# Optimization experiments

Hardware: AMD Instinct MI355X
Metric: run time of the kernel (lower is better)

Reference implementation:

```python
import jax, jax.numpy as jnp
import numpy as np

B, T, W, E, H, EMB, NVOCAB, WIN = 256, 200, 200, 768, 256, 32, 201, 8


def setup_inputs() -> dict:
    key = jax.random.key(0)
    ks = jax.random.split(key, 12)
    s = 0.05
    inputs = jax.random.normal(ks[0], (B, T, E), jnp.float32)
    full_word_embeddings = jax.random.normal(ks[1], (B, W, E), jnp.float32)
    lengths = jax.random.randint(ks[2], (B,), T // 2, T + 1)
    fix = jax.random.randint(ks[3], (B, T), 1, NVOCAB)
    fix_seq = jnp.where(jnp.arange(T)[None, :] < lengths[:, None], fix, 0)
    emb_table = (jax.random.normal(ks[4], (NVOCAB, EMB)) * s).at[0].set(0.0)  # padding_idx=0
    W_ih = jax.random.normal(ks[5], (3 * H, E + EMB)) * s  # torch GRU layout, gates r,z,n
    W_hh = jax.random.normal(ks[6], (3 * H, H)) * s
    b_ih = jax.random.normal(ks[7], (3 * H,)) * s
    b_hh = jax.random.normal(ks[8], (3 * H,)) * s
    W_out = jax.random.normal(ks[9], (E, H)) * s  # output_layer: Linear(H, E)
    b_out = jnp.zeros((E,), jnp.float32)
    W_dur = jax.random.normal(ks[10], (1, H)) * s  # duration_layer: Linear(H, 1)
    b_dur = jnp.zeros((1,), jnp.float32)
    return {"inputs": inputs, "fix_seq": fix_seq, "full_word_embeddings": full_word_embeddings,
            "lengths": lengths, "expert_id": 0, "emb_table": emb_table,
            "W_ih": W_ih, "b_ih": b_ih, "W_hh": W_hh, "b_hh": b_hh,
            "W_out": W_out, "b_out": b_out, "W_dur": W_dur, "b_dur": b_dur}


def _gru(x, W_ih, b_ih, W_hh, b_hh, h_dim):
    # x: [B,T,I]. Precompute input projections once, scan over time.
    xg = jnp.einsum('bti,gi->btg', x, W_ih) + b_ih  # [B,T,3H]

    def step(h, xg_t):
        hg = h @ W_hh.T + b_hh
        xr, xz, xn = jnp.split(xg_t, 3, axis=-1)
        hr, hz, hn = jnp.split(hg, 3, axis=-1)
        r = jax.nn.sigmoid(xr + hr)
        z = jax.nn.sigmoid(xz + hz)
        n = jnp.tanh(xn + r * hn)
        h_new = (1.0 - z) * n + z * h
        return h_new, h_new

    h0 = jnp.zeros((x.shape[0], h_dim), x.dtype)
    _, outs = jax.lax.scan(step, h0, jnp.swapaxes(xg, 0, 1))
    return jnp.swapaxes(outs, 0, 1)  # [B,T,H]


def reference(inputs, fix_seq, full_word_embeddings, lengths, expert_id,
              emb_table, W_ih, b_ih, W_hh, b_hh, W_out, b_out, W_dur, b_dur):
    del expert_id  # weights of the selected expert are passed directly
    valid_mask = fix_seq != 0
    scan_emb = emb_table[fix_seq]  # [B,T,32]
    rnn_in = jnp.concatenate([inputs, scan_emb], axis=-1)
    outputs = _gru(rnn_in, W_ih, b_ih, W_hh, b_hh, W_hh.shape[1])  # [B,T,H]
    # pad_packed_sequence zeros outputs beyond each sequence length
    tmask = jnp.arange(outputs.shape[1])[None, :] < lengths[:, None]
    outputs = outputs * tmask[..., None].astype(outputs.dtype)
    # dot attention: proj then scores against word embeddings
    proj = outputs @ W_out.T + b_out  # [B,T,E]
    logits = jnp.einsum('bte,bwe->btw', proj, full_word_embeddings)
    # saccade window mask around current fixation position
    wpos = jnp.arange(full_word_embeddings.shape[1])[None, None, :]
    dist = jnp.abs(wpos - fix_seq[..., None])
    sacc = (dist <= WIN) & valid_mask[..., None]
    logits = jnp.where(sacc, logits, -1e9)
    word_mask = jnp.sum(jnp.abs(full_word_embeddings), axis=-1) != 0
    logits = jnp.where(word_mask[:, None, :], logits, -1e9)
    dur_pred = (outputs @ W_dur.T + b_dur)[..., 0]  # [B,T]
    return logits, dur_pred
```

## Files before the change

kernel.cpp:

```cpp
#include <hip/hip_runtime.h>
#include <hip/hip_bf16.h>

typedef __attribute__((ext_vector_type(8))) short bf16x8;
typedef __attribute__((ext_vector_type(4))) float f32x4;
typedef __attribute__((ext_vector_type(4))) int   i32x4;

#define NB 256
#define NT 200
#define NW 200
#define NE 768
#define NH 256
#define NEMB 32
#define KIN 800
#define G3H 768
#define MROWS 51200

__device__ __forceinline__ float bf2f(unsigned short h) {
    return __uint_as_float(((unsigned)h) << 16);
}
__device__ __forceinline__ unsigned short f2bf(float f) {
    unsigned u = __float_as_uint(f);
    u += 0x7fff + ((u >> 16) & 1);
    return (unsigned short)(u >> 16);
}
__device__ __forceinline__ float sigm(float x) { return 1.0f / (1.0f + __expf(-x)); }
__device__ __forceinline__ float tanh_fast(float x) {
    float e = __expf(2.0f * x);
    return 1.0f - 2.0f / (e + 1.0f);
}

#if __has_builtin(__builtin_amdgcn_sdot4)
__device__ __forceinline__ int SDOT4(int a, int b, int c) {
    return __builtin_amdgcn_sdot4(a, b, c, false);
}
#else
__device__ __forceinline__ int SDOT4(int a, int b, int c) {
    #pragma unroll
    for (int j = 0; j < 4; j++)
        c += (int)(signed char)(a >> (8 * j)) * (int)(signed char)(b >> (8 * j));
    return c;
}
#endif

__device__ __forceinline__ void gload16(const void* g, void* l) {
    __builtin_amdgcn_global_load_lds((const __attribute__((address_space(1))) unsigned int*)g,
                                     (__attribute__((address_space(3))) unsigned int*)l,
                                     16, 0, 0);
}

__global__ void prep1(const float* __restrict__ inputs, const int* __restrict__ fix_seq,
                      const float* __restrict__ emb, const float* __restrict__ Wih,
                      const float* __restrict__ Wout, const float* __restrict__ bih,
                      const float* __restrict__ bhh,
                      unsigned short* __restrict__ Abf, unsigned short* __restrict__ Wihbf,
                      unsigned short* __restrict__ Woutbf, float* __restrict__ biasC) {
    const long gid0 = (long)blockIdx.x * blockDim.x + threadIdx.x;
    if (gid0 < G3H) biasC[gid0] = bih[gid0] + (gid0 < 512 ? bhh[gid0] : 0.0f);
    const long NA = (long)MROWS * 100;
    const long NWU = 768L * 100;
    const long NOU = 768L * 32;
    const long total = NA + NWU + NOU;
    for (long u = gid0; u < total; u += (long)gridDim.x * blockDim.x) {
        bf16x8 v;
        unsigned short* dst;
        if (u < NA) {
            long row = u / 100;
            int c8 = (int)(u % 100) * 8;
            const float* s;
            if (c8 < NE) {
                s = inputs + row * NE + c8;
            } else {
                int fx = fix_seq[row];
                s = emb + (long)fx * NEMB + (c8 - NE);
            }
            #pragma unroll
            for (int j = 0; j < 8; j++) v[j] = (short)f2bf(s[j]);
            dst = Abf + row * KIN + c8;
        } else if (u < NA + NWU) {
            long u2 = u - NA;
            long row = u2 / 100;
            int c8 = (int)(u2 % 100) * 8;
            const float* s = Wih + row * KIN + c8;
            #pragma unroll
            for (int j = 0; j < 8; j++) v[j] = (short)f2bf(s[j]);
            dst = Wihbf + row * KIN + c8;
        } else {
            long u3 = u - NA - NWU;
            long row = u3 / 32;
            int c8 = (int)(u3 % 32) * 8;
            const float* s = Wout + row * NH + c8;
            #pragma unroll
            for (int j = 0; j < 8; j++) v[j] = (short)f2bf(s[j]);
            dst = Woutbf + row * NH + c8;
        }
        *(bf16x8*)dst = v;
    }
}

__global__ __launch_bounds__(256)
void gemm_bt128(const unsigned short* __restrict__ A,
                const unsigned short* __restrict__ Bw,
                const float* __restrict__ bias,
                unsigned short* __restrict__ Out,
                int M, int N, int K) {
    __shared__ unsigned short As[128 * 32];
    __shared__ unsigned short Bs[128 * 32];
    const int bid = (int)((blockIdx.x & 7) * (gridDim.x >> 3) + (blockIdx.x >> 3));
    const int nblk = N >> 7;
    const int m0 = (bid / nblk) << 7;
    const int n0 = (bid % nblk) << 7;
    const int tid = threadIdx.x;
    const int lane = tid & 63;
    const int wave = tid >> 6;
    const int wm = (wave >> 1) << 6;
    const int wn = (wave & 1) << 6;
    const int nk = K >> 5;

    const int srow = tid >> 2;
    const int sseg = (tid & 3) << 4;
    const char* gA0 = (const char*)(A + (long)(m0 + srow) * K) + sseg;
    const char* gA1 = (const char*)(A + (long)(m0 + 64 + srow) * K) + sseg;
    const char* gB0 = (const char*)(Bw + (long)(n0 + srow) * K) + sseg;
    const char* gB1 = (const char*)(Bw + (long)(n0 + 64 + srow) * K) + sseg;
    char* lA0 = (char*)As + wave * 1024;
    char* lA1 = (char*)As + 4096 + wave * 1024;
    char* lB0 = (char*)Bs + wave * 1024;
    char* lB1 = (char*)Bs + 4096 + wave * 1024;

    f32x4 acc[4][4] = {};

    for (int kt = 0; kt < nk; kt++) {
        __syncthreads();
        gload16(gA0 + kt * 64, lA0);
        gload16(gA1 + kt * 64, lA1);
        gload16(gB0 + kt * 64, lB0);
        gload16(gB1 + kt * 64, lB1);
        asm volatile("s_waitcnt vmcnt(0)" ::: "memory");
        __syncthreads();
        bf16x8 af[4], bfr[4];
        #pragma unroll
        for (int mi = 0; mi < 4; mi++)
            af[mi] = *(const bf16x8*)((const char*)As +
                        (wm + mi * 16 + (lane & 15)) * 64 + ((lane >> 4) << 4));
        #pragma unroll
        for (int ni = 0; ni < 4; ni++)
            bfr[ni] = *(const bf16x8*)((const char*)Bs +
                        (wn + ni * 16 + (lane & 15)) * 64 + ((lane >> 4) << 4));
        #pragma unroll
        for (int mi = 0; mi < 4; mi++)
            #pragma unroll
            for (int ni = 0; ni < 4; ni++)
                acc[mi][ni] = __builtin_amdgcn_mfma_f32_16x16x32_bf16(
                                  af[mi], bfr[ni], acc[mi][ni], 0, 0, 0);
    }
    #pragma unroll
    for (int ni = 0; ni < 4; ni++) {
        const int col = n0 + wn + ni * 16 + (lane & 15);
        const float bv = bias[col];
        #pragma unroll
        for (int mi = 0; mi < 4; mi++) {
            const int row = m0 + wm + mi * 16 + ((lane >> 4) << 2);
            #pragma unroll
            for (int r = 0; r < 4; r++)
                Out[(long)(row + r) * N + col] = f2bf(acc[mi][ni][r] + bv);
        }
    }
}

__global__ __launch_bounds__(512, 2)
__attribute__((amdgpu_waves_per_eu(2, 2)))
void gru_scan(const unsigned short* __restrict__ xg,
              const float* __restrict__ Whh,
              const float* __restrict__ bhh,
              const int* __restrict__ lengths,
              unsigned short* __restrict__ hout) {
    __shared__ __align__(16) unsigned char h8[2][256];
    const int tid = threadIdx.x;
    const int lane = tid & 63;
    const int wave = tid >> 6;
    const int b = blockIdx.x;
    const int col = wave * 32 + (lane & 31);
    const int kh = lane >> 5;

    int W[3][32];
    #pragma unroll
    for (int g = 0; g < 3; g++) {
        const float* wr = Whh + (long)(g * 256 + col) * NH + kh * 128;
        #pragma unroll
        for (int d = 0; d < 32; d++) {
            const float4 f = *(const float4*)(wr + d * 4);
            unsigned pack = 0;
            #pragma unroll
            for (int j = 0; j < 4; j++) {
                const float fv = j == 0 ? f.x : j == 1 ? f.y : j == 2 ? f.z : f.w;
                int wq = (int)rintf(fv * 400.0f);
                wq = wq > 127 ? 127 : (wq < -127 ? -127 : wq);
                pack |= ((unsigned)(wq & 0xff)) << (8 * j);
            }
            W[g][d] = (int)pack;
        }
    }
    const float bhn = bhh[512 + col];
    const int len = lengths[b];
    if (tid < 128) ((unsigned*)h8)[tid] = 0u;

    const unsigned short* xrow = xg + (long)b * NT * G3H;
    unsigned short xv0 = xrow[col], xv1 = xrow[256 + col], xv2 = xrow[512 + col];
    float hp = 0.0f;
    const float ISC = 1.0f / (400.0f * 127.0f);
    const bool wlo = (lane < 32);

    asm volatile("s_waitcnt lgkmcnt(0)" ::: "memory");
    __builtin_amdgcn_sched_barrier(0);
    __builtin_amdgcn_s_barrier();
    __builtin_amdgcn_sched_barrier(0);

    for (int t = 0; t < NT; t++) {
        const unsigned char* hb = h8[(t + 1) & 1] + kh * 128;
        int p0a = 0, p0b = 0, p1a = 0, p1b = 0, p2a = 0, p2b = 0;
        #pragma unroll
        for (int r = 0; r < 8; r++) {
            const i32x4 hv = *(const i32x4*)(hb + r * 16);
            p0a = SDOT4(hv[0], W[0][r * 4 + 0], p0a);
            p1a = SDOT4(hv[0], W[1][r * 4 + 0], p1a);
            p2a = SDOT4(hv[0], W[2][r * 4 + 0], p2a);
            p0b = SDOT4(hv[1], W[0][r * 4 + 1], p0b);
            p1b = SDOT4(hv[1], W[1][r * 4 + 1], p1b);
            p2b = SDOT4(hv[1], W[2][r * 4 + 1], p2b);
            p0a = SDOT4(hv[2], W[0][r * 4 + 2], p0a);
            p1a = SDOT4(hv[2], W[1][r * 4 + 2], p1a);
            p2a = SDOT4(hv[2], W[2][r * 4 + 2], p2a);
            p0b = SDOT4(hv[3], W[0][r * 4 + 3], p0b);
            p1b = SDOT4(hv[3], W[1][r * 4 + 3], p1b);
            p2b = SDOT4(hv[3], W[2][r * 4 + 3], p2b);
        }
        int p0 = p0a + p0b, p1 = p1a + p1b, p2 = p2a + p2b;
        p0 += __shfl_xor(p0, 32);
        p1 += __shfl_xor(p1, 32);
        p2 += __shfl_xor(p2, 32);
        const float r = sigm(bf2f(xv0) + (float)p0 * ISC);
        const float z = sigm(bf2f(xv1) + (float)p1 * ISC);
        const float n = tanh_fast(bf2f(xv2) + r * ((float)p2 * ISC + bhn));
        hp = (1.0f - z) * n + z * hp;
        if (wlo) {
            h8[t & 1][col] = (unsigned char)((int)rintf(hp * 127.0f) & 0xff);
            hout[((long)b * NT + t) * NH + col] = (t < len) ? f2bf(hp) : (unsigned short)0;
        }
        if (t + 1 < NT) {
            const unsigned short* xn = xrow + (long)(t + 1) * G3H;
            xv0 = xn[col]; xv1 = xn[256 + col]; xv2 = xn[512 + col];
        }
        asm volatile("s_waitcnt lgkmcnt(0)" ::: "memory");
        __builtin_amdgcn_sched_barrier(0);
        __builtin_amdgcn_s_barrier();
        __builtin_amdgcn_sched_barrier(0);
    }
}

__global__ void prep2(const float* __restrict__ fwe, unsigned short* __restrict__ fwebf,
                      unsigned char* __restrict__ wmask) {
    const int row = (int)((blockIdx.x * blockDim.x + threadIdx.x) >> 6);
    const int lane = threadIdx.x & 63;
    if (row >= MROWS) return;
    const float* s = fwe + (long)row * NE;
    unsigned short* d = fwebf + (long)row * NE;
    float asum = 0.0f;
    #pragma unroll
    for (int i = 0; i < 12; i++) {
        const float v = s[lane + i * 64];
        asum += fabsf(v);
        d[lane + i * 64] = f2bf(v);
    }
    #pragma unroll
    for (int off = 32; off >= 1; off >>= 1) asum += __shfl_xor(asum, off);
    if (lane == 0) wmask[row] = (asum != 0.0f) ? 1 : 0;
}

__global__ void logits_gemm(const unsigned short* __restrict__ Aproj,
                            const unsigned short* __restrict__ Bfwe,
                            const int* __restrict__ fix_seq,
                            const unsigned char* __restrict__ wmask,
                            float* __restrict__ out) {
    __shared__ unsigned short As[64 * 32];
    __shared__ unsigned short Bs[64 * 32];
    const int blk = blockIdx.x;
    const int b = blk >> 4;
    const int mt = (blk >> 2) & 3;
    const int ntile = blk & 3;
    const int t0 = mt << 6;
    const int w0 = ntile << 6;
    const int tid = threadIdx.x;
    const int lane = tid & 63;
    const int wave = tid >> 6;
    const int wm = (wave >> 1) << 5;
    const int wn = (wave & 1) << 5;

    const int srow = tid >> 2;
    const int sbyte = (tid & 3) << 4;
    const int tA = t0 + srow > 199 ? 199 : t0 + srow;
    const int wB = w0 + srow > 199 ? 199 : w0 + srow;
    const char* ga = (const char*)(Aproj + ((long)b * NT + tA) * NE) + sbyte;
    const char* gb = (const char*)(Bfwe + ((long)b * NW + wB) * NE) + sbyte;
    char* la = (char*)As + srow * 64 + sbyte;
    char* lb = (char*)Bs + srow * 64 + sbyte;

    f32x4 acc[2][2] = {};
    bf16x8 ra = *(const bf16x8*)(ga);
    bf16x8 rb = *(const bf16x8*)(gb);
    for (int kt = 0; kt < 24; kt++) {
        __syncthreads();
        *(bf16x8*)(la) = ra;
        *(bf16x8*)(lb) = rb;
        __syncthreads();
        if (kt < 23) {
            ra = *(const bf16x8*)(ga + (kt + 1) * 64);
            rb = *(const bf16x8*)(gb + (kt + 1) * 64);
        }
        bf16x8 af[2], bfr[2];
        #pragma unroll
        for (int mi = 0; mi < 2; mi++)
            af[mi] = *(const bf16x8*)((const char*)As +
                        (wm + mi * 16 + (lane & 15)) * 64 + ((lane >> 4) << 4));
        #pragma unroll
        for (int ni = 0; ni < 2; ni++)
            bfr[ni] = *(const bf16x8*)((const char*)Bs +
                        (wn + ni * 16 + (lane & 15)) * 64 + ((lane >> 4) << 4));
        #pragma unroll
        for (int mi = 0; mi < 2; mi++)
            #pragma unroll
            for (int ni = 0; ni < 2; ni++)
                acc[mi][ni] = __builtin_amdgcn_mfma_f32_16x16x32_bf16(
                                  af[mi], bfr[ni], acc[mi][ni], 0, 0, 0);
    }
    #pragma unroll
    for (int mi = 0; mi < 2; mi++) {
        #pragma unroll
        for (int r = 0; r < 4; r++) {
            const int t = t0 + wm + mi * 16 + ((lane >> 4) << 2) + r;
            if (t >= NT) continue;
            const int fx = fix_seq[b * NT + t];
            #pragma unroll
            for (int ni = 0; ni < 2; ni++) {
                const int w = w0 + wn + ni * 16 + (lane & 15);
                if (w >= NW) continue;
                int d = w - fx; d = d < 0 ? -d : d;
                const bool ok = (fx != 0) && (d <= 8) && (wmask[b * NW + w] != 0);
                out[(long)b * (NT * NW) + t * NW + w] = ok ? acc[mi][ni][r] : -1e9f;
            }
        }
    }
}

__global__ void dur_kernel(const unsigned short* __restrict__ hout,
                           const float* __restrict__ Wdur, const float* __restrict__ bdur,
                           float* __restrict__ out) {
    const int row = (int)((blockIdx.x * blockDim.x + threadIdx.x) >> 6);
    const int lane = threadIdx.x & 63;
    if (row >= MROWS) return;
    const unsigned short* hp = hout + (long)row * NH + lane * 4;
    const uint2 hv = *(const uint2*)hp;
    const float4 wv = *(const float4*)(Wdur + lane * 4);
    float s = bf2f((unsigned short)(hv.x & 0xffff)) * wv.x
            + bf2f((unsigned short)(hv.x >> 16)) * wv.y
            + bf2f((unsigned short)(hv.y & 0xffff)) * wv.z
            + bf2f((unsigned short)(hv.y >> 16)) * wv.w;
    #pragma unroll
    for (int off = 32; off >= 1; off >>= 1) s += __shfl_down(s, off);
    if (lane == 0) out[(long)NB * NT * NW + row] = s + bdur[0];
}

extern "C" void kernel_launch(void* const* d_in, const int* in_sizes, int n_in,
                              void* d_out, int out_size, void* d_ws, size_t ws_size,
                              hipStream_t stream) {
    (void)in_sizes; (void)n_in; (void)out_size; (void)ws_size;
    const float* inputs  = (const float*)d_in[0];
    const int*   fix_seq = (const int*)d_in[1];
    const float* fwe     = (const float*)d_in[2];
    const int*   lengths = (const int*)d_in[3];
    const float* emb     = (const float*)d_in[5];
    const float* Wih     = (const float*)d_in[6];
    const float* bih     = (const float*)d_in[7];
    const float* Whh     = (const float*)d_in[8];
    const float* bhh     = (const float*)d_in[9];
    const float* Wout    = (const float*)d_in[10];
    const float* bout    = (const float*)d_in[11];
    const float* Wdur    = (const float*)d_in[12];
    const float* bdur    = (const float*)d_in[13];
    float* out = (float*)d_out;

    char* ws = (char*)d_ws;
    unsigned short* Abf    = (unsigned short*)(ws);
    unsigned short* xgbf   = (unsigned short*)(ws + 81920000);
    unsigned short* hout   = (unsigned short*)(ws + 160563200);
    unsigned short* Wihbf  = (unsigned short*)(ws + 186777600);
    unsigned short* Woutbf = (unsigned short*)(ws + 188006400);
    unsigned char*  wmask  = (unsigned char*)(ws + 188399616);
    float*          biasC  = (float*)(ws + 188450816);
    unsigned short* projbf = Abf;
    unsigned short* fwebf  = xgbf;

    prep1<<<2048, 256, 0, stream>>>(inputs, fix_seq, emb, Wih, Wout, bih, bhh,
                                    Abf, Wihbf, Woutbf, biasC);
    gemm_bt128<<<400 * 6, 256, 0, stream>>>(Abf, Wihbf, biasC, xgbf, MROWS, G3H, KIN);
    gru_scan<<<256, 512, 0, stream>>>(xgbf, Whh, bhh, lengths, hout);
    gemm_bt128<<<400 * 6, 256, 0, stream>>>(hout, Woutbf, bout, projbf, MROWS, G3H, NH);
    prep2<<<12800, 256, 0, stream>>>(fwe, fwebf, wmask);
    logits_gemm<<<4096, 256, 0, stream>>>(projbf, fwebf, fix_seq, wmask, out);
    dur_kernel<<<12800, 256, 0, stream>>>(hout, Wdur, bdur, out);
}
```

Measured before the change: 559.4 us.

## Reassociate attention projection onto word embeddings to shrink logits GEMM K

Rewrites logits = (h·W_outᵀ + b_out)·fweᵀ as h·(fwe·W_out)ᵀ + fwe·b_out. A GEMM now projects the word embeddings into H=256 space (fwe·W_out, N=256, K=768) in place of projecting GRU outputs to E=768, and the bias term becomes a per-word dot product computed in prep2. The logits GEMM then runs over K=256 instead of 768 and loads its tiles with direct global-to-LDS copies. This cuts projection FLOPs and logits-GEMM traffic. The cost is a transposed W_out conversion, an extra dvec buffer, and a slightly different rounding path through bf16 G.

```diff
diff --git a/kernel.cpp b/kernel.cpp
--- a/kernel.cpp
+++ b/kernel.cpp
@@ -53,12 +53,14 @@
                       const float* __restrict__ Wout, const float* __restrict__ bih,
                       const float* __restrict__ bhh,
                       unsigned short* __restrict__ Abf, unsigned short* __restrict__ Wihbf,
-                      unsigned short* __restrict__ Woutbf, float* __restrict__ biasC) {
+                      unsigned short* __restrict__ WoutTbf, float* __restrict__ biasC,
+                      float* __restrict__ bias0) {
     const long gid0 = (long)blockIdx.x * blockDim.x + threadIdx.x;
     if (gid0 < G3H) biasC[gid0] = bih[gid0] + (gid0 < 512 ? bhh[gid0] : 0.0f);
+    if (gid0 < NH) bias0[gid0] = 0.0f;
     const long NA = (long)MROWS * 100;
     const long NWU = 768L * 100;
-    const long NOU = 768L * 32;
+    const long NOU = 256L * 96;
     const long total = NA + NWU + NOU;
     for (long u = gid0; u < total; u += (long)gridDim.x * blockDim.x) {
         bf16x8 v;
@@ -86,12 +88,12 @@
             dst = Wihbf + row * KIN + c8;
         } else {
             long u3 = u - NA - NWU;
-            long row = u3 / 32;
-            int c8 = (int)(u3 % 32) * 8;
-            const float* s = Wout + row * NH + c8;
-            #pragma unroll
-            for (int j = 0; j < 8; j++) v[j] = (short)f2bf(s[j]);
-            dst = Woutbf + row * NH + c8;
+            long row = u3 / 96;
+            int c8 = (int)(u3 % 96) * 8;
+            #pragma unroll
+            for (int j = 0; j < 8; j++)
+                v[j] = (short)f2bf(Wout[(long)(c8 + j) * NH + row]);
+            dst = WoutTbf + row * NE + c8;
         }
         *(bf16x8*)dst = v;
     }
@@ -257,30 +259,40 @@
     }
 }
 
-__global__ void prep2(const float* __restrict__ fwe, unsigned short* __restrict__ fwebf,
-                      unsigned char* __restrict__ wmask) {
+__global__ void prep2(const float* __restrict__ fwe, const float* __restrict__ bout,
+                      unsigned short* __restrict__ fwebf,
+                      unsigned char* __restrict__ wmask, float* __restrict__ dvec) {
     const int row = (int)((blockIdx.x * blockDim.x + threadIdx.x) >> 6);
     const int lane = threadIdx.x & 63;
     if (row >= MROWS) return;
     const float* s = fwe + (long)row * NE;
     unsigned short* d = fwebf + (long)row * NE;
-    float asum = 0.0f;
+    float asum = 0.0f, vdot = 0.0f;
     #pragma unroll
     for (int i = 0; i < 12; i++) {
         const float v = s[lane + i * 64];
         asum += fabsf(v);
+        vdot += v * bout[lane + i * 64];
         d[lane + i * 64] = f2bf(v);
     }
     #pragma unroll
-    for (int off = 32; off >= 1; off >>= 1) asum += __shfl_xor(asum, off);
-    if (lane == 0) wmask[row] = (asum != 0.0f) ? 1 : 0;
-}
-
-__global__ void logits_gemm(const unsigned short* __restrict__ Aproj,
-                            const unsigned short* __restrict__ Bfwe,
-                            const int* __restrict__ fix_seq,
-                            const unsigned char* __restrict__ wmask,
-                            float* __restrict__ out) {
+    for (int off = 32; off >= 1; off >>= 1) {
+        asum += __shfl_xor(asum, off);
+        vdot += __shfl_xor(vdot, off);
+    }
+    if (lane == 0) {
+        wmask[row] = (asum != 0.0f) ? 1 : 0;
+        dvec[row] = vdot;
+    }
+}
+
+__global__ __launch_bounds__(256)
+void logits_gemm(const unsigned short* __restrict__ Hrow,
+                 const unsigned short* __restrict__ G,
+                 const int* __restrict__ fix_seq,
+                 const unsigned char* __restrict__ wmask,
+                 const float* __restrict__ dvec,
+                 float* __restrict__ out) {
     __shared__ unsigned short As[64 * 32];
     __shared__ unsigned short Bs[64 * 32];
     const int blk = blockIdx.x;
@@ -296,26 +308,21 @@
     const int wn = (wave & 1) << 5;
 
     const int srow = tid >> 2;
-    const int sbyte = (tid & 3) << 4;
+    const int sseg = (tid & 3) << 4;
     const int tA = t0 + srow > 199 ? 199 : t0 + srow;
     const int wB = w0 + srow > 199 ? 199 : w0 + srow;
-    const char* ga = (const char*)(Aproj + ((long)b * NT + tA) * NE) + sbyte;
-    const char* gb = (const char*)(Bfwe + ((long)b * NW + wB) * NE) + sbyte;
-    char* la = (char*)As + srow * 64 + sbyte;
-    char* lb = (char*)Bs + srow * 64 + sbyte;
+    const char* ga = (const char*)(Hrow + ((long)b * NT + tA) * NH) + sseg;
+    const char* gb = (const char*)(G + ((long)b * NW + wB) * NH) + sseg;
+    char* la = (char*)As + wave * 1024;
+    char* lb = (char*)Bs + wave * 1024;
 
     f32x4 acc[2][2] = {};
-    bf16x8 ra = *(const bf16x8*)(ga);
-    bf16x8 rb = *(const bf16x8*)(gb);
-    for (int kt = 0; kt < 24; kt++) {
+    for (int kt = 0; kt < 8; kt++) {
         __syncthreads();
-        *(bf16x8*)(la) = ra;
-        *(bf16x8*)(lb) = rb;
+        gload16(ga + kt * 64, la);
+        gload16(gb + kt * 64, lb);
+        asm volatile("s_waitcnt vmcnt(0)" ::: "memory");
         __syncthreads();
-        if (kt < 23) {
-            ra = *(const bf16x8*)(ga + (kt + 1) * 64);
-            rb = *(const bf16x8*)(gb + (kt + 1) * 64);
-        }
         bf16x8 af[2], bfr[2];
         #pragma unroll
         for (int mi = 0; mi < 2; mi++)
@@ -345,7 +352,8 @@
                 if (w >= NW) continue;
                 int d = w - fx; d = d < 0 ? -d : d;
                 const bool ok = (fx != 0) && (d <= 8) && (wmask[b * NW + w] != 0);
-                out[(long)b * (NT * NW) + t * NW + w] = ok ? acc[mi][ni][r] : -1e9f;
+                out[(long)b * (NT * NW) + t * NW + w] =
+                    ok ? acc[mi][ni][r] + dvec[b * NW + w] : -1e9f;
             }
         }
     }
@@ -389,22 +397,24 @@
     float* out = (float*)d_out;
 
     char* ws = (char*)d_ws;
-    unsigned short* Abf    = (unsigned short*)(ws);
-    unsigned short* xgbf   = (unsigned short*)(ws + 81920000);
-    unsigned short* hout   = (unsigned short*)(ws + 160563200);
-    unsigned short* Wihbf  = (unsigned short*)(ws + 186777600);
-    unsigned short* Woutbf = (unsigned short*)(ws + 188006400);
-    unsigned char*  wmask  = (unsigned char*)(ws + 188399616);
-    float*          biasC  = (float*)(ws + 188450816);
-    unsigned short* projbf = Abf;
-    unsigned short* fwebf  = xgbf;
+    unsigned short* Abf     = (unsigned short*)(ws);
+    unsigned short* xgbf    = (unsigned short*)(ws + 81920000);
+    unsigned short* hout    = (unsigned short*)(ws + 160563200);
+    unsigned short* Wihbf   = (unsigned short*)(ws + 186777600);
+    unsigned short* WoutTbf = (unsigned short*)(ws + 188006400);
+    unsigned char*  wmask   = (unsigned char*)(ws + 188399616);
+    float*          biasC   = (float*)(ws + 188450816);
+    float*          dvec    = (float*)(ws + 188453888);
+    float*          bias0   = (float*)(ws + 188658688);
+    unsigned short* fwebf   = Abf;
+    unsigned short* Gbf     = xgbf;
 
     prep1<<<2048, 256, 0, stream>>>(inputs, fix_seq, emb, Wih, Wout, bih, bhh,
-                                    Abf, Wihbf, Woutbf, biasC);
+                                    Abf, Wihbf, WoutTbf, biasC, bias0);
     gemm_bt128<<<400 * 6, 256, 0, stream>>>(Abf, Wihbf, biasC, xgbf, MROWS, G3H, KIN);
+    prep2<<<12800, 256, 0, stream>>>(fwe, bout, fwebf, wmask, dvec);
     gru_scan<<<256, 512, 0, stream>>>(xgbf, Whh, bhh, lengths, hout);
-    gemm_bt128<<<400 * 6, 256, 0, stream>>>(hout, Woutbf, bout, projbf, MROWS, G3H, NH);
-    prep2<<<12800, 256, 0, stream>>>(fwe, fwebf, wmask);
-    logits_gemm<<<4096, 256, 0, stream>>>(projbf, fwebf, fix_seq, wmask, out);
+    gemm_bt128<<<400 * 2, 256, 0, stream>>>(fwebf, WoutTbf, bias0, Gbf, MROWS, NH, NE);
+    logits_gemm<<<4096, 256, 0, stream>>>(hout, Gbf, fix_seq, wmask, dvec, out);
     dur_kernel<<<12800, 256, 0, stream>>>(hout, Wdur, bdur, out);
 }
```

New measurement: 522.1 us. 1.07x faster.
